# Performance work log

Hardware: AMD Instinct MI355X
Metric: run time of the kernel (lower is better)

Reference implementation:

```python
import jax, jax.numpy as jnp
import numpy as np

B, OBS, NH, LAT = 8192, 256, 2048, 128

def setup_inputs() -> dict:
    key = jax.random.key(0)
    k1, k2, k3, k4, k5, k6 = jax.random.split(key, 6)
    s1 = 1.0 / np.sqrt(OBS + NH)
    s2 = 1.0 / np.sqrt(NH)
    return {
        "x": jax.random.normal(k1, (B, OBS), dtype=jnp.float32),
        "h": jax.random.normal(k2, (B, NH), dtype=jnp.float32),
        "W_i2h": jax.random.normal(k3, (NH, OBS + NH), dtype=jnp.float32) * s1,
        "b_i2h": jax.random.normal(k4, (NH,), dtype=jnp.float32) * s1,
        "W_h2o": jax.random.normal(k5, (2 * LAT, NH), dtype=jnp.float32) * s2,
        "b_h2o": jax.random.normal(k6, (2 * LAT,), dtype=jnp.float32) * s2,
    }

def reference(x, h, W_i2h, b_i2h, W_h2o, b_h2o):
    # combined = cat((x, h), dim=1)  -> [B, OBS+NH]
    combined = jnp.concatenate([x, h], axis=1)
    # h_new = tanh(i2h(combined));  Linear is y = x @ W.T + b
    h_new = jnp.tanh(combined @ W_i2h.T + b_i2h)
    out = h_new @ W_h2o.T + b_h2o  # [B, 2*LAT]
    return (out, h_new)
```

## Files before the change

kernel.cpp:

```cpp
#include <hip/hip_runtime.h>
#include <hip/hip_bf16.h>
#include <cstdint>

using bf16 = __hip_bfloat16;
typedef __attribute__((ext_vector_type(8))) short short8;
typedef __attribute__((ext_vector_type(4))) float floatx4;

static constexpr int BATCH = 8192;
static constexpr int K1    = 2304;
static constexpr int N1    = 2048;
static constexpr int K2    = 2048;
static constexpr int N2    = 256;
static constexpr int KT1   = K1 / 64;

__device__ __forceinline__ void gload_lds16(const void* g, void* l) {
  __builtin_amdgcn_global_load_lds(
      (const __attribute__((address_space(1))) void*)g,
      (__attribute__((address_space(3))) void*)l, 16, 0, 0);
}

__device__ __forceinline__ float fast_tanh(float x) {
  float e = __builtin_amdgcn_exp2f(x * 2.8853900817779268f);
  return 1.0f - 2.0f * __builtin_amdgcn_rcpf(e + 1.0f);
}

__device__ __forceinline__ short8 cvt8(const float* src) {
  float4 a = ((const float4*)src)[0];
  float4 b = ((const float4*)src)[1];
  union { short8 v; bf16 e[8]; } u;
  u.e[0] = __float2bfloat16(a.x); u.e[1] = __float2bfloat16(a.y);
  u.e[2] = __float2bfloat16(a.z); u.e[3] = __float2bfloat16(a.w);
  u.e[4] = __float2bfloat16(b.x); u.e[5] = __float2bfloat16(b.y);
  u.e[6] = __float2bfloat16(b.z); u.e[7] = __float2bfloat16(b.w);
  return u.v;
}

static constexpr int SEG0 = BATCH * (K1 / 8);
static constexpr int SEG1 = N1 * K1 / 8;
static constexpr int SEG2 = N2 * K2 / 8;
static constexpr int SEG3 = BATCH * (N2 / 4);
__global__ __launch_bounds__(256) void prep(
    const float* __restrict__ x, const float* __restrict__ h,
    const float* __restrict__ W1, const float* __restrict__ W2,
    const float* __restrict__ b2,
    bf16* __restrict__ comb, bf16* __restrict__ W1b, bf16* __restrict__ W2b,
    float* __restrict__ outp) {
  int i = blockIdx.x * 256 + threadIdx.x;
  if (i < SEG0) {
    int row  = i / 288;
    int slot = i - row * 288;
    const float* src = (slot < 32) ? (x + (size_t)row * 256 + slot * 8)
                                   : (h + (size_t)row * 2048 + (slot - 32) * 8);
    *(short8*)(comb + (size_t)row * 2304 + slot * 8) = cvt8(src);
  } else if (i < SEG0 + SEG1) {
    int j = i - SEG0;
    *(short8*)(W1b + (size_t)j * 8) = cvt8(W1 + (size_t)j * 8);
  } else if (i < SEG0 + SEG1 + SEG2) {
    int j = i - (SEG0 + SEG1);
    *(short8*)(W2b + (size_t)j * 8) = cvt8(W2 + (size_t)j * 8);
  } else {
    int j = i - (SEG0 + SEG1 + SEG2);
    float4 b = ((const float4*)b2)[j & 63];
    ((float4*)outp)[j] = b;
  }
}

__global__ __launch_bounds__(512, 2) void gemm1_tanh(
    const bf16* __restrict__ A, const bf16* __restrict__ W,
    const float* __restrict__ bias,
    float* __restrict__ hf32, bf16* __restrict__ hb16) {
  __shared__ bf16 lds[2][2][2][8192];
  const int t    = threadIdx.x;
  const int lane = t & 63;
  const int wave = t >> 6;
  const int wm   = (wave >> 2) * 128;
  const int wn   = (wave & 3) * 64;
  const int quad = lane >> 4;
  const int r15  = lane & 15;

  const int swz   = ((quad ^ ((r15 >> 1) & 3)) << 4);
  const int baseA = wm * 64 + r15 * 64 + swz;
  const int baseB = 32768 + wn * 64 + r15 * 64 + swz;

  const int srow  = t >> 2;
  const int sslot = t & 3;
  const int sq    = (sslot ^ ((srow >> 1) & 3)) * 8;

  const size_t Abase = (size_t)blockIdx.x * 256 * K1;
  const size_t Bbase = (size_t)blockIdx.y * 256 * K1;
  const size_t gA0 = Abase + (size_t)srow * K1 + sq;
  const size_t gA1 = Abase + (size_t)(srow + 128) * K1 + sq;
  const size_t gB0 = Bbase + (size_t)srow * K1 + sq;
  const size_t gB1 = Bbase + (size_t)(srow + 128) * K1 + sq;
  const int d0 = t * 16, d1 = 8192 + t * 16;
  char* const ldsb = (char*)lds;

#define STG(sb, mat_, skh, skt) do {                                         \
    const int ktc_ = ((skt) < KT1 ? (skt) : (KT1 - 1));                      \
    const size_t ko_ = (size_t)ktc_ * 64 + (skh) * 32;                       \
    char* const la_ = ldsb + ((sb) << 16) + ((mat_) * 32768) + ((skh) << 14);\
    const bf16* g0_ = (mat_) ? (W + gB0 + ko_) : (A + gA0 + ko_);            \
    const bf16* g1_ = (mat_) ? (W + gB1 + ko_) : (A + gA1 + ko_);            \
    gload_lds16(g0_, la_ + d0);                                              \
    gload_lds16(g1_, la_ + d1);                                              \
  } while (0)

  floatx4 acc[8][4];
  const floatx4 z = {0.f, 0.f, 0.f, 0.f};
#pragma unroll
  for (int i = 0; i < 8; i++)
#pragma unroll
    for (int j = 0; j < 4; j++) acc[i][j] = z;

  short8 afA[4], afB[4], bfA[4], bfB[4];

  STG(0, 0, 0, 0); STG(0, 1, 0, 0);
  STG(0, 0, 1, 0); STG(0, 1, 1, 0);
  STG(1, 0, 0, 1); STG(1, 1, 0, 1);
  asm volatile("s_waitcnt vmcnt(8)" ::: "memory");
  __builtin_amdgcn_s_barrier();
  __builtin_amdgcn_sched_barrier(0);
  {
#pragma unroll
    for (int mt = 0; mt < 4; ++mt)
      afA[mt] = *(const short8*)(ldsb + baseA + mt * 1024);
#pragma unroll
    for (int nt = 0; nt < 4; ++nt)
      bfA[nt] = *(const short8*)(ldsb + baseB + nt * 1024);
  }

#define PH(ccb, cks, cmtg, AFC, BFC, rcb, rks, rmtg, AFN, BFN, RB,           \
           sb, smat, skh, skt, VMW, LGS) do {                                \
    const char* Lr_ = ldsb + ((rcb) << 16) + ((rks) << 14);                  \
    _Pragma("unroll")                                                        \
    for (int mt = 0; mt < 4; ++mt)                                           \
      AFN[mt] = *(const short8*)(Lr_ + baseA + (rmtg) * 4096 + mt * 1024);   \
    if (RB) {                                                                \
      _Pragma("unroll")                                                      \
      for (int nt = 0; nt < 4; ++nt)                                         \
        BFN[nt] = *(const short8*)(Lr_ + baseB + nt * 1024);                 \
    }                                                                        \
    STG(sb, smat, skh, skt);                                                 \
    __builtin_amdgcn_sched_barrier(0);                                       \
    if (VMW) asm volatile("s_waitcnt vmcnt(6)" ::: "memory");                \
    asm volatile("s_waitcnt lgkmcnt(" LGS ")" ::: "memory");                 \
    __builtin_amdgcn_sched_barrier(0);                                       \
    __builtin_amdgcn_s_setprio(1);                                           \
    _Pragma("unroll")                                                        \
    for (int mt = 0; mt < 4; ++mt)                                           \
      _Pragma("unroll")                                                      \
      for (int nt = 0; nt < 4; ++nt)                                         \
        acc[(cmtg) * 4 + mt][nt] = __builtin_amdgcn_mfma_f32_16x16x32_bf16(  \
            AFC[mt], BFC[nt], acc[(cmtg) * 4 + mt][nt], 0, 0, 0);            \
    __builtin_amdgcn_s_setprio(0);                                           \
    __builtin_amdgcn_s_barrier();                                            \
    __builtin_amdgcn_sched_barrier(0);                                       \
  } while (0)

#pragma clang loop unroll(disable)
  for (int t2 = 0; t2 < KT1 / 2; ++t2) {
    const int n = 2 * t2;
    PH(0, 0, 0, afA, bfA,  0, 0, 1, afB, bfB, 0,  1, 0, 1, n + 1, 1, "4");
    PH(0, 0, 1, afB, bfA,  0, 1, 0, afA, bfB, 1,  1, 1, 1, n + 1, 0, "8");
    PH(0, 1, 0, afA, bfB,  0, 1, 1, afB, bfA, 0,  0, 0, 0, n + 2, 1, "4");
    PH(0, 1, 1, afB, bfB,  1, 0, 0, afA, bfA, 1,  0, 1, 0, n + 2, 0, "8");
    PH(1, 0, 0, afA, bfA,  1, 0, 1, afB, bfB, 0,  0, 0, 1, n + 2, 1, "4");
    PH(1, 0, 1, afB, bfA,  1, 1, 0, afA, bfB, 1,  0, 1, 1, n + 2, 0, "8");
    PH(1, 1, 0, afA, bfB,  1, 1, 1, afB, bfA, 0,  1, 0, 0, n + 3, 1, "4");
    PH(1, 1, 1, afB, bfB,  0, 0, 0, afA, bfA, 1,  1, 1, 0, n + 3, 0, "8");
  }
#undef PH
#undef STG

  const int gcol0 = blockIdx.y * 256 + wn;
  float bv[4];
#pragma unroll
  for (int nt = 0; nt < 4; ++nt) bv[nt] = bias[gcol0 + nt * 16 + r15];
  const size_t grow0 = (size_t)blockIdx.x * 256 + wm;
#pragma unroll
  for (int mt = 0; mt < 8; ++mt) {
#pragma unroll
    for (int i = 0; i < 4; ++i) {
      const size_t gr = grow0 + mt * 16 + quad * 4 + i;
      const size_t rb = gr * (size_t)N1;
#pragma unroll
      for (int nt = 0; nt < 4; ++nt) {
        const int gc = gcol0 + nt * 16 + r15;
        float v = fast_tanh(acc[mt][nt][i] + bv[nt]);
        hf32[rb + gc] = v;
        hb16[rb + gc] = __float2bfloat16(v);
      }
    }
  }
}

__global__ __launch_bounds__(256) void gemm2_out(
    const bf16* __restrict__ A, const bf16* __restrict__ W,
    float* __restrict__ out) {
  __shared__ bf16 As[2][32 * 64];
  __shared__ bf16 Bs[2][256 * 64];
  const int t    = threadIdx.x;
  const int lane = t & 63;
  const int wave = t >> 6;
  const int quad = lane >> 4;
  const int r15  = lane & 15;
  const int srow = t >> 3;
  const int sc   = t & 7;

  const int mrow0 = blockIdx.x * 32;
  const int kbase = blockIdx.y * (K2 / 2);

#define G2STAGE(b, kt) do {                                                  \
    const int k0_ = kbase + (kt) * 64;                                       \
    {                                                                        \
      int gc_ = k0_ + ((sc ^ (srow & 7)) << 3);                              \
      gload_lds16(A + (size_t)(mrow0 + srow) * K2 + gc_,                     \
                  (char*)As[b] + t * 16);                                    \
    }                                                                        \
    _Pragma("unroll")                                                        \
    for (int it = 0; it < 8; ++it) {                                         \
      int row_ = it * 32 + srow;                                             \
      int gc_  = k0_ + ((sc ^ (row_ & 7)) << 3);                             \
      gload_lds16(W + (size_t)row_ * K2 + gc_,                               \
                  (char*)Bs[b] + it * 4096 + t * 16);                        \
    }                                                                        \
  } while (0)

  floatx4 acc[2][4];
  const floatx4 z = {0.f, 0.f, 0.f, 0.f};
#pragma unroll
  for (int i = 0; i < 2; i++)
#pragma unroll
    for (int j = 0; j < 4; j++) acc[i][j] = z;

  G2STAGE(0, 0);
#pragma clang loop unroll(disable)
  for (int kt = 0; kt < 16; ++kt) {
    const int cur = kt & 1;
    if (kt + 1 < 16) {
      G2STAGE(cur ^ 1, kt + 1);
      asm volatile("s_waitcnt vmcnt(9)" ::: "memory");
    } else {
      asm volatile("s_waitcnt vmcnt(0)" ::: "memory");
    }
    __builtin_amdgcn_s_barrier();
    asm volatile("" ::: "memory");
#pragma unroll
    for (int ks = 0; ks < 2; ++ks) {
      short8 af[2], bfr[4];
      const int kq = ks * 4 + quad;
#pragma unroll
      for (int mt = 0; mt < 2; ++mt) {
        int row = mt * 16 + r15;
        af[mt] = *(const short8*)((const char*)As[cur] + row * 128 +
                                  ((kq ^ (row & 7)) << 4));
      }
#pragma unroll
      for (int nt = 0; nt < 4; ++nt) {
        int row = wave * 64 + nt * 16 + r15;
        bfr[nt] = *(const short8*)((const char*)Bs[cur] + row * 128 +
                                   ((kq ^ (row & 7)) << 4));
      }
#pragma unroll
      for (int mt = 0; mt < 2; ++mt)
#pragma unroll
        for (int nt = 0; nt < 4; ++nt)
          acc[mt][nt] = __builtin_amdgcn_mfma_f32_16x16x32_bf16(
              af[mt], bfr[nt], acc[mt][nt], 0, 0, 0);
    }
    asm volatile("" ::: "memory");
    __builtin_amdgcn_s_barrier();
  }
#undef G2STAGE

  const int gcol0 = wave * 64;
#pragma unroll
  for (int mt = 0; mt < 2; ++mt) {
#pragma unroll
    for (int i = 0; i < 4; ++i) {
      size_t gr = (size_t)mrow0 + mt * 16 + quad * 4 + i;
      size_t rb = gr * (size_t)N2;
#pragma unroll
      for (int nt = 0; nt < 4; ++nt) {
        int gc = gcol0 + nt * 16 + r15;
        unsafeAtomicAdd(&out[rb + gc], acc[mt][nt][i]);
      }
    }
  }
}

extern "C" void kernel_launch(void* const* d_in, const int* in_sizes, int n_in,
                              void* d_out, int out_size, void* d_ws,
                              size_t ws_size, hipStream_t stream) {
  const float* x     = (const float*)d_in[0];
  const float* h     = (const float*)d_in[1];
  const float* W_i2h = (const float*)d_in[2];
  const float* b_i2h = (const float*)d_in[3];
  const float* W_h2o = (const float*)d_in[4];
  const float* b_h2o = (const float*)d_in[5];

  float* out       = (float*)d_out;
  float* hnew_f32  = out + (size_t)BATCH * N2;

  bf16* comb   = (bf16*)d_ws;
  bf16* Wi2h_b = comb + (size_t)BATCH * K1;
  bf16* Wh2o_b = Wi2h_b + (size_t)N1 * K1;
  bf16* hnew_b = Wh2o_b + (size_t)N2 * K2;

  prep<<<(SEG0 + SEG1 + SEG2 + SEG3) / 256, 256, 0, stream>>>(
      x, h, W_i2h, W_h2o, b_h2o, comb, Wi2h_b, Wh2o_b, out);

  gemm1_tanh<<<dim3(BATCH / 256, N1 / 256), 512, 0, stream>>>(
      comb, Wi2h_b, b_i2h, hnew_f32, hnew_b);

  gemm2_out<<<dim3(BATCH / 32, 2), 256, 0, stream>>>(hnew_b, Wh2o_b, out);
}
```

Baseline: 256.1 us.

## Fuse second GEMM into first GEMM epilogue with per-column-block partial sums

The h2o GEMM now runs inside the i2h GEMM epilogue. Each block stages its tanh output tile as bf16 in LDS and multiplies it by the matching 256-column K-slice of W_h2o, with B fragments read straight from global memory. This removes the bf16 h_new round trip through global memory and the separate gemm2 launch. When the workspace is large enough, partial outputs go to 8 slabs that a small reduce kernel sums with the bias; otherwise they are accumulated with atomics. The cost is heavier epilogue work per block, uncached global loads of W2, and an extra partial-sum buffer and pass.

```diff
diff --git a/kernel.cpp b/kernel.cpp
--- a/kernel.cpp
+++ b/kernel.cpp
@@ -65,11 +65,26 @@
   }
 }
 
+__global__ __launch_bounds__(256) void reduce8(
+    const float* __restrict__ part, const float* __restrict__ bias,
+    float* __restrict__ out) {
+  int i = blockIdx.x * 256 + threadIdx.x;
+  float4 s = ((const float4*)bias)[i & 63];
+#pragma unroll
+  for (int b = 0; b < 8; ++b) {
+    float4 p = ((const float4*)(part + (size_t)b * BATCH * N2))[i];
+    s.x += p.x; s.y += p.y; s.z += p.z; s.w += p.w;
+  }
+  ((float4*)out)[i] = s;
+}
+
+template <int MODE>
 __global__ __launch_bounds__(512, 2) void gemm1_tanh(
     const bf16* __restrict__ A, const bf16* __restrict__ W,
-    const float* __restrict__ bias,
-    float* __restrict__ hf32, bf16* __restrict__ hb16) {
-  __shared__ bf16 lds[2][2][2][8192];
+    const float* __restrict__ bias, const bf16* __restrict__ W2b,
+    float* __restrict__ hf32, float* __restrict__ outp) {
+  __shared__ __align__(16) char ldsb_s[131072];
+  char* const ldsb = ldsb_s;
   const int t    = threadIdx.x;
   const int lane = t & 63;
   const int wave = t >> 6;
@@ -93,7 +108,6 @@
   const size_t gB0 = Bbase + (size_t)srow * K1 + sq;
   const size_t gB1 = Bbase + (size_t)(srow + 128) * K1 + sq;
   const int d0 = t * 16, d1 = 8192 + t * 16;
-  char* const ldsb = (char*)lds;
 
 #define STG(sb, mat_, skh, skt) do {                                         \
     const int ktc_ = ((skt) < KT1 ? (skt) : (KT1 - 1));                      \
@@ -172,118 +186,79 @@
 #undef PH
 #undef STG
 
+  asm volatile("s_waitcnt vmcnt(0) lgkmcnt(0)" ::: "memory");
+  __builtin_amdgcn_s_barrier();
+  __builtin_amdgcn_sched_barrier(0);
+
   const int gcol0 = blockIdx.y * 256 + wn;
   float bv[4];
 #pragma unroll
   for (int nt = 0; nt < 4; ++nt) bv[nt] = bias[gcol0 + nt * 16 + r15];
   const size_t grow0 = (size_t)blockIdx.x * 256 + wm;
+
+#define HB(row, col) ((row) * 512 + (((((col) >> 3) ^ ((row) & 7))) << 4) + \
+                      (((col) & 7) << 1))
+#pragma unroll
+  for (int mt = 0; mt < 8; ++mt) {
+#pragma unroll
+    for (int i = 0; i < 4; ++i) {
+      const int lrow = wm + mt * 16 + quad * 4 + i;
+      const size_t rb = (grow0 + mt * 16 + quad * 4 + i) * (size_t)N1;
+#pragma unroll
+      for (int nt = 0; nt < 4; ++nt) {
+        const int lcol = wn + nt * 16 + r15;
+        float v = fast_tanh(acc[mt][nt][i] + bv[nt]);
+        hf32[rb + gcol0 - wn + lcol] = v;
+        *(bf16*)(ldsb + HB(lrow, lcol)) = __float2bfloat16(v);
+      }
+    }
+  }
+  asm volatile("s_waitcnt lgkmcnt(0)" ::: "memory");
+  __builtin_amdgcn_s_barrier();
+  __builtin_amdgcn_sched_barrier(0);
+
+#pragma unroll
+  for (int i = 0; i < 8; i++)
+#pragma unroll
+    for (int j = 0; j < 4; j++) acc[i][j] = z;
+
+  const bf16* w2base = W2b + (size_t)blockIdx.y * 256;
+#pragma unroll
+  for (int ks = 0; ks < 8; ++ks) {
+    short8 bq[4], aq[8];
+#pragma unroll
+    for (int nt = 0; nt < 4; ++nt)
+      bq[nt] = *(const short8*)(w2base + (size_t)(wn + nt * 16 + r15) * 2048 +
+                                ks * 32 + quad * 8);
+#pragma unroll
+    for (int mt = 0; mt < 8; ++mt) {
+      const int row = wm + mt * 16 + r15;
+      aq[mt] = *(const short8*)(ldsb + row * 512 +
+                                ((((ks * 4 + quad) ^ (row & 7))) << 4));
+    }
+#pragma unroll
+    for (int mt = 0; mt < 8; ++mt)
+#pragma unroll
+      for (int nt = 0; nt < 4; ++nt)
+        acc[mt][nt] = __builtin_amdgcn_mfma_f32_16x16x32_bf16(
+            aq[mt], bq[nt], acc[mt][nt], 0, 0, 0);
+  }
+#undef HB
+
+  const size_t slab = (MODE == 1) ? (size_t)blockIdx.y * BATCH * N2 : 0;
 #pragma unroll
   for (int mt = 0; mt < 8; ++mt) {
 #pragma unroll
     for (int i = 0; i < 4; ++i) {
       const size_t gr = grow0 + mt * 16 + quad * 4 + i;
-      const size_t rb = gr * (size_t)N1;
 #pragma unroll
       for (int nt = 0; nt < 4; ++nt) {
-        const int gc = gcol0 + nt * 16 + r15;
-        float v = fast_tanh(acc[mt][nt][i] + bv[nt]);
-        hf32[rb + gc] = v;
-        hb16[rb + gc] = __float2bfloat16(v);
-      }
-    }
-  }
-}
-
-__global__ __launch_bounds__(256) void gemm2_out(
-    const bf16* __restrict__ A, const bf16* __restrict__ W,
-    float* __restrict__ out) {
-  __shared__ bf16 As[2][32 * 64];
-  __shared__ bf16 Bs[2][256 * 64];
-  const int t    = threadIdx.x;
-  const int lane = t & 63;
-  const int wave = t >> 6;
-  const int quad = lane >> 4;
-  const int r15  = lane & 15;
-  const int srow = t >> 3;
-  const int sc   = t & 7;
-
-  const int mrow0 = blockIdx.x * 32;
-  const int kbase = blockIdx.y * (K2 / 2);
-
-#define G2STAGE(b, kt) do {                                                  \
-    const int k0_ = kbase + (kt) * 64;                                       \
-    {                                                                        \
-      int gc_ = k0_ + ((sc ^ (srow & 7)) << 3);                              \
-      gload_lds16(A + (size_t)(mrow0 + srow) * K2 + gc_,                     \
-                  (char*)As[b] + t * 16);                                    \
-    }                                                                        \
-    _Pragma("unroll")                                                        \
-    for (int it = 0; it < 8; ++it) {                                         \
-      int row_ = it * 32 + srow;                                             \
-      int gc_  = k0_ + ((sc ^ (row_ & 7)) << 3);                             \
-      gload_lds16(W + (size_t)row_ * K2 + gc_,                               \
-                  (char*)Bs[b] + it * 4096 + t * 16);                        \
-    }                                                                        \
-  } while (0)
-
-  floatx4 acc[2][4];
-  const floatx4 z = {0.f, 0.f, 0.f, 0.f};
-#pragma unroll
-  for (int i = 0; i < 2; i++)
-#pragma unroll
-    for (int j = 0; j < 4; j++) acc[i][j] = z;
-
-  G2STAGE(0, 0);
-#pragma clang loop unroll(disable)
-  for (int kt = 0; kt < 16; ++kt) {
-    const int cur = kt & 1;
-    if (kt + 1 < 16) {
-      G2STAGE(cur ^ 1, kt + 1);
-      asm volatile("s_waitcnt vmcnt(9)" ::: "memory");
-    } else {
-      asm volatile("s_waitcnt vmcnt(0)" ::: "memory");
-    }
-    __builtin_amdgcn_s_barrier();
-    asm volatile("" ::: "memory");
-#pragma unroll
-    for (int ks = 0; ks < 2; ++ks) {
-      short8 af[2], bfr[4];
-      const int kq = ks * 4 + quad;
-#pragma unroll
-      for (int mt = 0; mt < 2; ++mt) {
-        int row = mt * 16 + r15;
-        af[mt] = *(const short8*)((const char*)As[cur] + row * 128 +
-                                  ((kq ^ (row & 7)) << 4));
-      }
-#pragma unroll
-      for (int nt = 0; nt < 4; ++nt) {
-        int row = wave * 64 + nt * 16 + r15;
-        bfr[nt] = *(const short8*)((const char*)Bs[cur] + row * 128 +
-                                   ((kq ^ (row & 7)) << 4));
-      }
-#pragma unroll
-      for (int mt = 0; mt < 2; ++mt)
-#pragma unroll
-        for (int nt = 0; nt < 4; ++nt)
-          acc[mt][nt] = __builtin_amdgcn_mfma_f32_16x16x32_bf16(
-              af[mt], bfr[nt], acc[mt][nt], 0, 0, 0);
-    }
-    asm volatile("" ::: "memory");
-    __builtin_amdgcn_s_barrier();
-  }
-#undef G2STAGE
-
-  const int gcol0 = wave * 64;
-#pragma unroll
-  for (int mt = 0; mt < 2; ++mt) {
-#pragma unroll
-    for (int i = 0; i < 4; ++i) {
-      size_t gr = (size_t)mrow0 + mt * 16 + quad * 4 + i;
-      size_t rb = gr * (size_t)N2;
-#pragma unroll
-      for (int nt = 0; nt < 4; ++nt) {
-        int gc = gcol0 + nt * 16 + r15;
-        unsafeAtomicAdd(&out[rb + gc], acc[mt][nt][i]);
+        const int gc = wn + nt * 16 + r15;
+        if (MODE == 0) {
+          unsafeAtomicAdd(&outp[gr * N2 + gc], acc[mt][nt][i]);
+        } else {
+          outp[slab + gr * N2 + gc] = acc[mt][nt][i];
+        }
       }
     }
   }
@@ -305,13 +280,21 @@
   bf16* comb   = (bf16*)d_ws;
   bf16* Wi2h_b = comb + (size_t)BATCH * K1;
   bf16* Wh2o_b = Wi2h_b + (size_t)N1 * K1;
-  bf16* hnew_b = Wh2o_b + (size_t)N2 * K2;
+  float* part  = (float*)(Wh2o_b + (size_t)N2 * K2);
+
+  const size_t ws_needed = (size_t)BATCH * K1 * 2 + (size_t)N1 * K1 * 2 +
+                           (size_t)N2 * K2 * 2 + (size_t)8 * BATCH * N2 * 4;
+  const bool big_ws = ws_size >= ws_needed;
 
   prep<<<(SEG0 + SEG1 + SEG2 + SEG3) / 256, 256, 0, stream>>>(
       x, h, W_i2h, W_h2o, b_h2o, comb, Wi2h_b, Wh2o_b, out);
 
-  gemm1_tanh<<<dim3(BATCH / 256, N1 / 256), 512, 0, stream>>>(
-      comb, Wi2h_b, b_i2h, hnew_f32, hnew_b);
-
-  gemm2_out<<<dim3(BATCH / 32, 2), 256, 0, stream>>>(hnew_b, Wh2o_b, out);
-}
+  if (big_ws) {
+    gemm1_tanh<1><<<dim3(BATCH / 256, N1 / 256), 512, 0, stream>>>(
+        comb, Wi2h_b, b_i2h, Wh2o_b, hnew_f32, part);
+    reduce8<<<(BATCH * N2 / 4) / 256, 256, 0, stream>>>(part, b_h2o, out);
+  } else {
+    gemm1_tanh<0><<<dim3(BATCH / 256, N1 / 256), 512, 0, stream>>>(
+        comb, Wi2h_b, b_i2h, Wh2o_b, hnew_f32, out);
+  }
+}
```

Result: no change. 255.5 us (-0.2%).
